# Kernel optimization log

Measured on AMD Instinct MI355X. Metric: run time of the kernel, lower is better.

## Reference

```python
import jax, jax.numpy as jnp
import numpy as np

N, B, E, H, D, L, NT = 30000, 16, 60000, 128, 64, 2, 5


def _build_graph():
    rng = np.random.default_rng(0)
    ng = N // B
    row = rng.integers(0, N, size=E)
    g = row // ng
    col = g * ng + rng.integers(0, ng, size=E)  # bonds stay within a graph
    order = np.argsort(g, kind='stable')        # sort bonds by graph id
    row, col = row[order], col[order]
    edge_index = np.stack([row, col]).astype(np.int32)
    # bond graph: bonds adjacent iff they share an atom (vectorized _build_bond_graph)
    atoms = np.concatenate([row, col])
    bonds = np.concatenate([np.arange(E), np.arange(E)])
    o2 = np.argsort(atoms, kind='stable')
    sb = bonds[o2]
    counts = np.bincount(atoms, minlength=N)
    offs = np.concatenate([[0], np.cumsum(counts)[:-1]])
    sq = counts * counts
    total = int(sq.sum())
    gid = np.repeat(np.arange(N), sq)
    poff = np.concatenate([[0], np.cumsum(sq)[:-1]])
    pos = np.arange(total) - np.repeat(poff, sq)
    c, o = counts[gid], offs[gid]
    ii, jj = pos // c, pos % c
    mask = ii != jj
    bond_edge_index = np.stack([sb[o + ii][mask], sb[o + jj][mask]]).astype(np.int32)
    batch = np.repeat(np.arange(B), ng).astype(np.int32)
    return edge_index, bond_edge_index, batch


def setup_inputs() -> dict:
    edge_index, bond_edge_index, batch = _build_graph()
    key = jax.random.key(0)
    ks = jax.random.split(key, 16)
    s = 0.05
    n = lambda k, shp: jax.random.normal(k, shp, jnp.float32) * s
    return {
        'atom_features': jax.random.normal(ks[0], (N, H), jnp.float32),
        'atom_pos': jax.random.normal(ks[1], (N, 3), jnp.float32),
        'atomic_numbers': jax.random.randint(ks[2], (N,), 1, 20, jnp.int32),
        'batch': jnp.asarray(batch),
        'edge_index': jnp.asarray(edge_index),
        'bond_edge_index': jnp.asarray(bond_edge_index),
        'iw1': n(ks[3], (2 * H, D)), 'ib1': jnp.zeros((D,), jnp.float32),
        'iw2': n(ks[4], (D, D)), 'ib2': jnp.zeros((D,), jnp.float32),
        'emb': n(ks[5], (L, NT, D)),
        'mw1': n(ks[6], (L, 3 * D, D)), 'mb1': jnp.zeros((L, D), jnp.float32),
        'mw2': n(ks[7], (L, D, D)), 'mb2': jnp.zeros((L, D), jnp.float32),
        'uw1': n(ks[8], (L, 2 * D, D)), 'ub1': jnp.zeros((L, D), jnp.float32),
        'uw2': n(ks[9], (L, D, D)), 'ub2': jnp.zeros((L, D), jnp.float32),
        'num_graphs': B,
    }


def reference(atom_features, atom_pos, iw1, ib1, iw2, ib2, emb, mw1, mb1, mw2, mb2,
              uw1, ub1, uw2, ub2, atomic_numbers, batch, edge_index, bond_edge_index,
              num_graphs):
    row, col = edge_index
    hi, hj = atom_features[row], atom_features[col]  # [E, H] gathers
    # bond_init MLP
    x = jax.nn.silu(jnp.concatenate([hi, hj], -1) @ iw1 + ib1) @ iw2 + ib2  # [E, D]
    # _classify_bonds: cosine-similarity thresholds (order matters, matches torch)
    ni = jnp.maximum(jnp.linalg.norm(hi, axis=-1), 1e-8)
    nj = jnp.maximum(jnp.linalg.norm(hj, axis=-1), 1e-8)
    sim = jnp.sum(hi * hj, -1) / (ni * nj)
    bt = jnp.where(sim > 0.8, 1, 0)
    bt = jnp.where(sim > 0.9, 2, bt)
    bt = jnp.where(sim < 0.3, 3, bt)
    src, dst = bond_edge_index  # x_j = x[src], x_i = x[dst]; aggregate at dst
    nb = x.shape[0]
    deg = jax.ops.segment_sum(jnp.ones(src.shape, jnp.float32), dst, num_segments=nb)
    denom = jnp.maximum(deg, 1.0)[:, None]  # PyG mean aggr: 0 for isolated nodes
    for l in range(mw1.shape[0]):
        te = emb[l][bt]  # [E, D] bond-type embedding
        msg_in = jnp.concatenate([x[dst], x[src], te[dst]], -1)  # [BE, 3D]
        msg = jax.nn.silu(msg_in @ mw1[l] + mb1[l]) @ mw2[l] + mb2[l]
        aggr = jax.ops.segment_sum(msg, dst, num_segments=nb) / denom
        upd_in = jnp.concatenate([aggr, x], -1)
        x = x + jax.nn.silu(upd_in @ uw1[l] + ub1[l]) @ uw2[l] + ub2[l]
    # pooling: edges are sorted by graph, so repeat_interleave == batch[row]
    bond_batch = batch[row]
    cnt = jax.ops.segment_sum(jnp.ones((nb,), jnp.float32), bond_batch, num_segments=num_graphs)
    gfeat = jax.ops.segment_sum(x, bond_batch, num_segments=num_graphs) / jnp.maximum(cnt, 1.0)[:, None]
    return x, gfeat
```

## Files before the change

### kernel.cpp

```cpp
#include <hip/hip_runtime.h>
#include <cstdint>
#include <cstddef>

#define HDIM 128
#define DDIM 64
#define NTYPES 5
#define NGRAPHS 16
#define PCHUNK 128
#define EPB 64
#define APW 8

typedef __attribute__((ext_vector_type(8))) short short8;
typedef __attribute__((ext_vector_type(4))) float f32x4;

static __device__ __forceinline__ short8 as_s8(uint4 u) {
    return __builtin_bit_cast(short8, u);
}

static __device__ __forceinline__ float silu_f(float v) {
    return v * __builtin_amdgcn_rcpf(1.0f + __expf(-v));
}

static __device__ __forceinline__ float4 ld4(const float* p) {
    return *reinterpret_cast<const float4*>(p);
}

static __device__ __forceinline__ void st4(float* p, float4 v) {
    *reinterpret_cast<float4*>(p) = v;
}

static __device__ __forceinline__ float4 add4(float4 a, float4 b) {
    return make_float4(a.x + b.x, a.y + b.y, a.z + b.z, a.w + b.w);
}

static __device__ __forceinline__ void silu_acc4(float4& s, float4 v) {
    s.x += silu_f(v.x);
    s.y += silu_f(v.y);
    s.z += silu_f(v.z);
    s.w += silu_f(v.w);
}

static __device__ __forceinline__ unsigned int bf16r(float f) {
    unsigned int u = __float_as_uint(f);
    return (u + 0x7FFFu + ((u >> 16) & 1u)) >> 16;
}
static __device__ __forceinline__ uint4 pack8(const float* f) {
    uint4 r;
    r.x = bf16r(f[0]) | (bf16r(f[1]) << 16);
    r.y = bf16r(f[2]) | (bf16r(f[3]) << 16);
    r.z = bf16r(f[4]) | (bf16r(f[5]) << 16);
    r.w = bf16r(f[6]) | (bf16r(f[7]) << 16);
    return r;
}
static __device__ __forceinline__ void unpack8(uint4 u, float4& a, float4& b) {
    a.x = __uint_as_float(u.x << 16);
    a.y = __uint_as_float(u.x & 0xFFFF0000u);
    a.z = __uint_as_float(u.y << 16);
    a.w = __uint_as_float(u.y & 0xFFFF0000u);
    b.x = __uint_as_float(u.z << 16);
    b.y = __uint_as_float(u.z & 0xFFFF0000u);
    b.z = __uint_as_float(u.w << 16);
    b.w = __uint_as_float(u.w & 0xFFFF0000u);
}

static __device__ __forceinline__ void hilo8(const float* f, uint4& h, uint4& lo) {
    h = pack8(f);
    float4 a, b;
    unpack8(h, a, b);
    float g[8] = {f[0] - a.x, f[1] - a.y, f[2] - a.z, f[3] - a.w,
                  f[4] - b.x, f[5] - b.y, f[6] - b.z, f[7] - b.w};
    lo = pack8(g);
}

static __device__ __forceinline__ int xcd_logical_block() {
    int chunk = (int)(gridDim.x >> 3);
    return (int)(blockIdx.x & 7) * chunk + (int)(blockIdx.x >> 3);
}

__global__ void __launch_bounds__(256) count_k(const int* __restrict__ bdst,
                                               int* __restrict__ cnt, int BE) {
    int i = blockIdx.x * 256 + threadIdx.x;
    if (i < BE)
        __hip_atomic_fetch_add(&cnt[bdst[i]], 1, __ATOMIC_RELAXED, __HIP_MEMORY_SCOPE_AGENT);
}

__global__ void __launch_bounds__(256) bsum_k(const int* __restrict__ cnt,
                                              int* __restrict__ bsum, int E) {
    __shared__ int red[256];
    int t = threadIdx.x;
    int i = blockIdx.x * 256 + t;
    red[t] = (i < E) ? cnt[i] : 0;
    __syncthreads();
    #pragma unroll
    for (int off = 128; off > 0; off >>= 1) {
        if (t < off) red[t] += red[t + off];
        __syncthreads();
    }
    if (t == 0) bsum[blockIdx.x] = red[0];
}

__global__ void __launch_bounds__(1024) bscan_k(const int* __restrict__ bsum,
                                                int* __restrict__ bpre, int NB) {
    __shared__ int sh[1024];
    int t = threadIdx.x;
    int v0 = (t < NB) ? bsum[t] : 0;
    sh[t] = v0;
    __syncthreads();
    for (int off = 1; off < 1024; off <<= 1) {
        int v = (t >= off) ? sh[t - off] : 0;
        __syncthreads();
        sh[t] += v;
        __syncthreads();
    }
    if (t < NB) bpre[t] = sh[t] - v0;
}

__global__ void __launch_bounds__(256) offs_k(const int* __restrict__ cnt,
                                              const int* __restrict__ bpre,
                                              int* __restrict__ offs,
                                              int* __restrict__ cursor, int E) {
    __shared__ int sh[256];
    int t = threadIdx.x;
    int i = blockIdx.x * 256 + t;
    int v0 = (i < E) ? cnt[i] : 0;
    sh[t] = v0;
    __syncthreads();
    for (int off = 1; off < 256; off <<= 1) {
        int v = (t >= off) ? sh[t - off] : 0;
        __syncthreads();
        sh[t] += v;
        __syncthreads();
    }
    int ex = sh[t] - v0 + bpre[blockIdx.x];
    if (i < E) { offs[i] = ex; cursor[i] = ex; }
    if (i == E - 1) offs[E] = ex + v0;
}

__global__ void __launch_bounds__(256) scatter_k(const int* __restrict__ bsrc,
                                                 const int* __restrict__ bdst,
                                                 int* __restrict__ cursor,
                                                 int* __restrict__ srclist, int BE) {
    int i = blockIdx.x * 256 + threadIdx.x;
    if (i < BE) {
        int d = bdst[i];
        int p = __hip_atomic_fetch_add(&cursor[d], 1, __ATOMIC_RELAXED,
                                       __HIP_MEMORY_SCOPE_AGENT);
        srclist[p] = bsrc[i];
    }
}

__global__ void __launch_bounds__(64) tt2_k(const float* __restrict__ emb,
                                            const float* __restrict__ mw1,
                                            const float* __restrict__ mb1,
                                            float* __restrict__ tt) {
    int b = blockIdx.x;
    int l = b / NTYPES, t = b % NTYPES, j = threadIdx.x;
    const float* embl = emb + (size_t)l * NTYPES * DDIM + (size_t)t * DDIM;
    const float* w1 = mw1 + (size_t)l * 192 * DDIM;
    float s = mb1[l * DDIM + j];
    #pragma unroll 8
    for (int k = 0; k < DDIM; ++k)
        s = fmaf(embl[k], w1[(HDIM + k) * DDIM + j], s);
    tt[(size_t)b * DDIM + j] = s;
}

__global__ void __launch_bounds__(64) fuse_k(const float* __restrict__ mw2,
                                             const float* __restrict__ mb2,
                                             const float* __restrict__ uw1,
                                             float* __restrict__ w2u,
                                             float* __restrict__ b2u) {
    int l = blockIdx.x >> 6, k = blockIdx.x & 63, j = threadIdx.x;
    const float* w2 = mw2 + (size_t)l * DDIM * DDIM;
    const float* u1 = uw1 + (size_t)l * 128 * DDIM;
    float s = 0.f;
    #pragma unroll 8
    for (int t = 0; t < DDIM; ++t)
        s = fmaf(w2[k * DDIM + t], u1[(size_t)t * DDIM + j], s);
    w2u[(size_t)l * DDIM * DDIM + (size_t)k * DDIM + j] = s;
    if (k == 0) {
        float b = 0.f;
        #pragma unroll 8
        for (int t = 0; t < DDIM; ++t)
            b = fmaf(mb2[l * DDIM + t], u1[(size_t)t * DDIM + j], b);
        b2u[l * DDIM + j] = b;
    }
}

__global__ void __launch_bounds__(64) packall_k(const float* __restrict__ w2u,
                                                const float* __restrict__ uw1,
                                                const float* __restrict__ uw2,
                                                const float* __restrict__ mw1,
                                                const float* __restrict__ iw2,
                                                uint4* __restrict__ fw2u,
                                                uint4* __restrict__ fu1b,
                                                uint4* __restrict__ fu2,
                                                uint4* __restrict__ fp,
                                                uint4* __restrict__ fiw2,
                                                uint4* __restrict__ fp0) {
    int b = blockIdx.x;
    int mat = b >> 3, jt = (b >> 1) & 3, ks = b & 1, l = threadIdx.x;
    const float* src;
    uint4* dst;
    switch (mat) {
        case 0: src = w2u;                         dst = fw2u;        break;
        case 1: src = w2u + 4096;                  dst = fw2u + 1024; break;
        case 2: src = uw1 + 64 * 64;               dst = fu1b;        break;
        case 3: src = uw1 + 128 * 64 + 64 * 64;    dst = fu1b + 1024; break;
        case 4: src = uw2;                         dst = fu2;         break;
        case 5: src = uw2 + 4096;                  dst = fu2 + 1024;  break;
        case 6: src = mw1 + (size_t)192 * 64;      dst = fp;          break;
        case 7: src = mw1 + (size_t)192 * 64 + 64 * 64; dst = fp + 1024; break;
        case 8: src = iw2;                         dst = fiw2;        break;
        case 9: src = mw1;                         dst = fp0;         break;
        default: src = mw1 + (size_t)64 * 64;      dst = fp0 + 1024;  break;
    }
    int k0 = ks * 32 + (l >> 4) * 8;
    int j = jt * 16 + (l & 15);
    float f[8];
    #pragma unroll
    for (int i = 0; i < 8; ++i) f[i] = src[(size_t)(k0 + i) * 64 + j];
    uint4 h, lo;
    hilo8(f, h, lo);
    size_t di = ((size_t)(jt * 2 + ks) * 64 + l) * 2;
    dst[di] = h;
    dst[di + 1] = lo;
}

static __device__ __forceinline__ int slotIdx(int row, int slot) {
    return row * 8 + (slot ^ (row & 7));
}

static __device__ __forceinline__ short8 ldFragA(const uint4* buf, int rowBase, int lane, int ks) {
    int row = rowBase + (lane & 15);
    int slot = ks * 4 + (lane >> 4);
    return as_s8(buf[slotIdx(row, slot)]);
}

static __device__ __forceinline__ void loadB(const uint4* __restrict__ frag, int jt, int lane,
                                             short8& h0, short8& h1, short8& l0, short8& l1) {
    const uint4* p0 = frag + ((size_t)(jt * 2 + 0) * 64 + lane) * 2;
    const uint4* p1 = frag + ((size_t)(jt * 2 + 1) * 64 + lane) * 2;
    h0 = as_s8(p0[0]); l0 = as_s8(p0[1]);
    h1 = as_s8(p1[0]); l1 = as_s8(p1[1]);
}

static __device__ __forceinline__ f32x4 gemm_tile(const uint4* Ahi, const uint4* Alo,
        int rowBase, int lane,
        short8 bh0, short8 bh1, short8 bl0, short8 bl1, f32x4 acc) {
    short8 ah0 = ldFragA(Ahi, rowBase, lane, 0);
    short8 ah1 = ldFragA(Ahi, rowBase, lane, 1);
    short8 al0 = ldFragA(Alo, rowBase, lane, 0);
    short8 al1 = ldFragA(Alo, rowBase, lane, 1);
    acc = __builtin_amdgcn_mfma_f32_16x16x32_bf16(ah0, bh0, acc, 0, 0, 0);
    acc = __builtin_amdgcn_mfma_f32_16x16x32_bf16(ah1, bh1, acc, 0, 0, 0);
    acc = __builtin_amdgcn_mfma_f32_16x16x32_bf16(al0, bh0, acc, 0, 0, 0);
    acc = __builtin_amdgcn_mfma_f32_16x16x32_bf16(al1, bh1, acc, 0, 0, 0);
    acc = __builtin_amdgcn_mfma_f32_16x16x32_bf16(ah0, bl0, acc, 0, 0, 0);
    acc = __builtin_amdgcn_mfma_f32_16x16x32_bf16(ah1, bl1, acc, 0, 0, 0);
    return acc;
}

__global__ void __launch_bounds__(256) atom_proj_k(
    const float* __restrict__ AF, const float* __restrict__ iw1,
    float* __restrict__ pa, float* __restrict__ qa, float* __restrict__ na, int N) {
    int lane = threadIdx.x & 63;
    int w = __builtin_amdgcn_readfirstlane((int)(threadIdx.x >> 6));
    int abase = blockIdx.x * (4 * APW) + w * APW;
    if (abase >= N) return;

    float accp[APW], accq[APW], nrm[APW];
    #pragma unroll
    for (int a = 0; a < APW; ++a) { accp[a] = 0.f; accq[a] = 0.f; nrm[a] = 0.f; }

    #pragma unroll 4
    for (int k = 0; k < HDIM; k += 4) {
        float wt[4], wb[4];
        #pragma unroll
        for (int kk = 0; kk < 4; ++kk) {
            wt[kk] = iw1[(size_t)(k + kk) * DDIM + lane];
            wb[kk] = iw1[(size_t)(HDIM + k + kk) * DDIM + lane];
        }
        #pragma unroll
        for (int a = 0; a < APW; ++a) {
            int aa = min(abase + a, N - 1);
            float4 hv = ld4(AF + (size_t)aa * HDIM + k);
            accp[a] = fmaf(hv.x, wt[0], accp[a]);
            accp[a] = fmaf(hv.y, wt[1], accp[a]);
            accp[a] = fmaf(hv.z, wt[2], accp[a]);
            accp[a] = fmaf(hv.w, wt[3], accp[a]);
            accq[a] = fmaf(hv.x, wb[0], accq[a]);
            accq[a] = fmaf(hv.y, wb[1], accq[a]);
            accq[a] = fmaf(hv.z, wb[2], accq[a]);
            accq[a] = fmaf(hv.w, wb[3], accq[a]);
            nrm[a] = fmaf(hv.x, hv.x, nrm[a]);
            nrm[a] = fmaf(hv.y, hv.y, nrm[a]);
            nrm[a] = fmaf(hv.z, hv.z, nrm[a]);
            nrm[a] = fmaf(hv.w, hv.w, nrm[a]);
        }
    }
    #pragma unroll
    for (int a = 0; a < APW; ++a) {
        int atom = abase + a;
        if (atom < N) {
            pa[(size_t)atom * DDIM + lane] = accp[a];
            qa[(size_t)atom * DDIM + lane] = accq[a];
            if (lane == 0) na[atom] = sqrtf(nrm[a]);
        }
    }
}

__global__ void __launch_bounds__(512, 4) bond_init2_k(
    const float* __restrict__ AF, const int* __restrict__ row, const int* __restrict__ col,
    const float* __restrict__ pa, const float* __restrict__ qa, const float* __restrict__ na,
    const float* __restrict__ b1, const uint4* __restrict__ fW2, const float* __restrict__ b2,
    const uint4* __restrict__ fP0,
    float* __restrict__ x, int* __restrict__ bt,
    float* __restrict__ pd, uint4* __restrict__ ps, int E) {
    __shared__ uint4 sAhi[512];
    __shared__ uint4 sAlo[512];
    __shared__ uint4 sXhi[512];
    __shared__ uint4 sXlo[512];
    int nEB = (E + EPB - 1) / EPB;
    int lb = xcd_logical_block();
    if (lb >= nEB) return;
    int tid = threadIdx.x;
    int lane = tid & 63;
    int w = __builtin_amdgcn_readfirstlane((int)(tid >> 6));
    int e0 = lb * EPB;

    {
        int dl = tid >> 3, q = tid & 7;
        int d = e0 + dl;
        bool ok = d < E;
        int dd = ok ? d : 0;
        int r = row[dd], c = col[dd];
        int jq = q * 8;

        const float* hi = AF + (size_t)r * HDIM + q * 16;
        const float* hj = AF + (size_t)c * HDIM + q * 16;
        float dt = 0.f;
        #pragma unroll
        for (int k = 0; k < 16; k += 4) {
            float4 a4 = ld4(hi + k), b4 = ld4(hj + k);
            dt += a4.x * b4.x + a4.y * b4.y + a4.z * b4.z + a4.w * b4.w;
        }
        dt += __shfl_xor(dt, 1, 64);
        dt += __shfl_xor(dt, 2, 64);
        dt += __shfl_xor(dt, 4, 64);
        if (q == 0 && ok) {
            float nr = fmaxf(na[r], 1e-8f), nc = fmaxf(na[c], 1e-8f);
            float sim = dt / (nr * nc);
            int t = 0;
            if (sim > 0.8f) t = 1;
            if (sim > 0.9f) t = 2;
            if (sim < 0.3f) t = 3;
            bt[d] = t;
        }

        const float* pr = pa + (size_t)r * DDIM + jq;
        const float* qc = qa + (size_t)c * DDIM + jq;
        float4 p0 = ld4(pr + 0), p1 = ld4(pr + 4);
        float4 q0 = ld4(qc + 0), q1 = ld4(qc + 4);
        float hv[8];
        hv[0] = silu_f(p0.x + q0.x + b1[jq + 0]);
        hv[1] = silu_f(p0.y + q0.y + b1[jq + 1]);
        hv[2] = silu_f(p0.z + q0.z + b1[jq + 2]);
        hv[3] = silu_f(p0.w + q0.w + b1[jq + 3]);
        hv[4] = silu_f(p1.x + q1.x + b1[jq + 4]);
        hv[5] = silu_f(p1.y + q1.y + b1[jq + 5]);
        hv[6] = silu_f(p1.z + q1.z + b1[jq + 6]);
        hv[7] = silu_f(p1.w + q1.w + b1[jq + 7]);
        if (!ok) {
            #pragma unroll
            for (int i = 0; i < 8; ++i) hv[i] = 0.f;
        }
        uint4 h4, l4;
        hilo8(hv, h4, l4);
        int si = slotIdx(dl, q);
        sAhi[si] = h4; sAlo[si] = l4;
    }
    int jt = w & 3, mh = w >> 2;
    short8 W2h0, W2h1, W2l0, W2l1;
    loadB(fW2, jt, lane, W2h0, W2h1, W2l0, W2l1);
    __syncthreads();

    int rb0 = mh * 32, rb1 = mh * 32 + 16;
    f32x4 z4 = {0.f, 0.f, 0.f, 0.f};
    f32x4 acc0 = z4, acc1 = z4;
    acc0 = gemm_tile(sAhi, sAlo, rb0, lane, W2h0, W2h1, W2l0, W2l1, acc0);
    acc1 = gemm_tile(sAhi, sAlo, rb1, lane, W2h0, W2h1, W2l0, W2l1, acc1);
    int j = jt * 16 + (lane & 15);
    float b2j = b2[j];
    unsigned short* hX = (unsigned short*)sXhi;
    unsigned short* lX = (unsigned short*)sXlo;
    #pragma unroll
    for (int r = 0; r < 4; ++r) {
        int rowi = rb0 + (lane >> 4) * 4 + r;
        int e = e0 + rowi;
        float xn = acc0[r] + b2j;
        if (e < E) x[(size_t)e * DDIM + j] = xn;
        unsigned int hb = bf16r(xn);
        float lov = xn - __uint_as_float(hb << 16);
        int ui = (rowi * 8 + ((j >> 3) ^ (rowi & 7))) * 8 + (j & 7);
        hX[ui] = (unsigned short)hb;
        lX[ui] = (unsigned short)bf16r(lov);
    }
    #pragma unroll
    for (int r = 0; r < 4; ++r) {
        int rowi = rb1 + (lane >> 4) * 4 + r;
        int e = e0 + rowi;
        float xn = acc1[r] + b2j;
        if (e < E) x[(size_t)e * DDIM + j] = xn;
        unsigned int hb = bf16r(xn);
        float lov = xn - __uint_as_float(hb << 16);
        int ui = (rowi * 8 + ((j >> 3) ^ (rowi & 7))) * 8 + (j & 7);
        hX[ui] = (unsigned short)hb;
        lX[ui] = (unsigned short)bf16r(lov);
    }
    __syncthreads();

    const uint4* fPw = (w < 4) ? fP0 : (fP0 + 1024);
    int jp = w & 3;
    short8 Ph0, Ph1, Pl0, Pl1;
    loadB(fPw, jp, lane, Ph0, Ph1, Pl0, Pl1);
    f32x4 q0 = z4, q1 = z4, q2 = z4, q3 = z4;
    q0 = gemm_tile(sXhi, sXlo, 0,  lane, Ph0, Ph1, Pl0, Pl1, q0);
    q1 = gemm_tile(sXhi, sXlo, 16, lane, Ph0, Ph1, Pl0, Pl1, q1);
    q2 = gemm_tile(sXhi, sXlo, 32, lane, Ph0, Ph1, Pl0, Pl1, q2);
    q3 = gemm_tile(sXhi, sXlo, 48, lane, Ph0, Ph1, Pl0, Pl1, q3);
    unsigned short* hA = (unsigned short*)sAhi;
    if (w < 4) {
        int jd = jp * 16 + (lane & 15);
        #pragma unroll
        for (int mt = 0; mt < 4; ++mt) {
            f32x4 qq = (mt == 0) ? q0 : (mt == 1) ? q1 : (mt == 2) ? q2 : q3;
            #pragma unroll
            for (int r = 0; r < 4; ++r) {
                int rowi = mt * 16 + (lane >> 4) * 4 + r;
                int e = e0 + rowi;
                if (e < E) pd[(size_t)e * DDIM + jd] = qq[r];
            }
        }
    } else {
        int js = jp * 16 + (lane & 15);
        #pragma unroll
        for (int mt = 0; mt < 4; ++mt) {
            f32x4 qq = (mt == 0) ? q0 : (mt == 1) ? q1 : (mt == 2) ? q2 : q3;
            #pragma unroll
            for (int r = 0; r < 4; ++r) {
                int rowi = mt * 16 + (lane >> 4) * 4 + r;
                int ui = (rowi * 8 + ((js >> 3) ^ (rowi & 7))) * 8 + (js & 7);
                hA[ui] = (unsigned short)bf16r(qq[r]);
            }
        }
    }
    __syncthreads();
    {
        int dl = tid >> 3, q = tid & 7;
        int d = e0 + dl;
        if (d < E) ps[(size_t)d * 8 + q] = sAhi[slotIdx(dl, q)];
    }
}

__global__ void __launch_bounds__(256) proj_k(const float* __restrict__ x,
                                              const float* __restrict__ w1 ,
                                              float* __restrict__ pd, uint4* __restrict__ ps,
                                              int E) {
    int lane = threadIdx.x & 63;
    int w = __builtin_amdgcn_readfirstlane((int)(threadIdx.x >> 6));
    int e = blockIdx.x * EPB + lane;
    bool ok = e < E;
    int eidx = ok ? e : 0;
    int j0 = w * 16;
    const float* xr = x + (size_t)eidx * DDIM;

    float apd[16], aps[16];
    #pragma unroll
    for (int jj = 0; jj < 16; ++jj) { apd[jj] = 0.f; aps[jj] = 0.f; }
    #pragma unroll 2
    for (int c = 0; c < 16; ++c) {
        float4 v = ld4(xr + c * 4);
        float xv[4] = {v.x, v.y, v.z, v.w};
        #pragma unroll
        for (int kk = 0; kk < 4; ++kk) {
            int k = c * 4 + kk;
            const float* wd = w1 + (size_t)k * DDIM + j0;
            const float* wsv = w1 + (size_t)(DDIM + k) * DDIM + j0;
            #pragma unroll
            for (int jj = 0; jj < 16; ++jj) {
                apd[jj] = fmaf(xv[kk], wd[jj], apd[jj]);
                aps[jj] = fmaf(xv[kk], wsv[jj], aps[jj]);
            }
        }
    }
    if (ok) {
        float* pr = pd + (size_t)e * DDIM + j0;
        st4(pr + 0,  make_float4(apd[0],  apd[1],  apd[2],  apd[3]));
        st4(pr + 4,  make_float4(apd[4],  apd[5],  apd[6],  apd[7]));
        st4(pr + 8,  make_float4(apd[8],  apd[9],  apd[10], apd[11]));
        st4(pr + 12, make_float4(apd[12], apd[13], apd[14], apd[15]));
        ps[(size_t)e * 8 + 2 * w + 0] = pack8(aps + 0);
        ps[(size_t)e * 8 + 2 * w + 1] = pack8(aps + 8);
    }
}

__global__ void __launch_bounds__(512, 4) layer_k(
    float* __restrict__ x, const float* __restrict__ pd, const uint4* __restrict__ ps,
    const float* __restrict__ tt_l, const int* __restrict__ bt,
    const int* __restrict__ offs, const int* __restrict__ srclist,
    const int* __restrict__ cnt,
    const uint4* __restrict__ fW2u, const float* __restrict__ b2u,
    const uint4* __restrict__ fU1b, const float* __restrict__ ub1,
    const uint4* __restrict__ fU2, const float* __restrict__ ub2,
    const uint4* __restrict__ fP ,
    float* __restrict__ pdn, uint4* __restrict__ psn, int E) {
    __shared__ uint4 sAhi[512];
    __shared__ uint4 sAlo[512];
    __shared__ uint4 sXhi[512];
    __shared__ uint4 sXlo[512];
    __shared__ float degLDS[64];
    int nEB = (E + EPB - 1) / EPB;
    int lb = xcd_logical_block();
    if (lb >= nEB) return;
    int tid = threadIdx.x;
    int lane = tid & 63;
    int w = __builtin_amdgcn_readfirstlane((int)(tid >> 6));
    int e0 = lb * EPB;

    {
        int dl = tid >> 3, q = tid & 7;
        int d = e0 + dl;
        bool ok = d < E;
        int dd = ok ? d : 0;
        int jq = q * 8;
        const float* xr = x + (size_t)dd * DDIM + jq;
        float4 xv0 = ld4(xr + 0), xv1 = ld4(xr + 4);
        int dc = cnt[dd];
        const float* pr = pd + (size_t)dd * DDIM + jq;
        const float* tp = tt_l + (size_t)bt[dd] * DDIM + jq;
        float4 b0 = add4(ld4(pr + 0), ld4(tp + 0));
        float4 b1 = add4(ld4(pr + 4), ld4(tp + 4));
        float4 s0 = make_float4(0, 0, 0, 0), s1 = s0;
        int p0 = ok ? offs[d] : 0, p1 = ok ? offs[d + 1] : 0;
        int p = p0;
        for (; p + 4 <= p1; p += 4) {
            uint4 u0 = ps[(size_t)srclist[p + 0] * 8 + q];
            uint4 u1 = ps[(size_t)srclist[p + 1] * 8 + q];
            uint4 u2 = ps[(size_t)srclist[p + 2] * 8 + q];
            uint4 u3 = ps[(size_t)srclist[p + 3] * 8 + q];
            float4 a, b;
            unpack8(u0, a, b);
            silu_acc4(s0, add4(b0, a));
            silu_acc4(s1, add4(b1, b));
            unpack8(u1, a, b);
            silu_acc4(s0, add4(b0, a));
            silu_acc4(s1, add4(b1, b));
            unpack8(u2, a, b);
            silu_acc4(s0, add4(b0, a));
            silu_acc4(s1, add4(b1, b));
            unpack8(u3, a, b);
            silu_acc4(s0, add4(b0, a));
            silu_acc4(s1, add4(b1, b));
        }
        for (; p < p1; ++p) {
            uint4 u0 = ps[(size_t)srclist[p] * 8 + q];
            float4 a, b;
            unpack8(u0, a, b);
            silu_acc4(s0, add4(b0, a));
            silu_acc4(s1, add4(b1, b));
        }
        float inv = 1.0f / fmaxf((float)dc, 1.0f);
        float sv[8] = {s0.x * inv, s0.y * inv, s0.z * inv, s0.w * inv,
                       s1.x * inv, s1.y * inv, s1.z * inv, s1.w * inv};
        float xf[8] = {xv0.x, xv0.y, xv0.z, xv0.w, xv1.x, xv1.y, xv1.z, xv1.w};
        if (!ok) {
            #pragma unroll
            for (int i = 0; i < 8; ++i) { sv[i] = 0.f; xf[i] = 0.f; }
        }
        uint4 h4, l4;
        int si = slotIdx(dl, q);
        hilo8(sv, h4, l4);
        sAhi[si] = h4; sAlo[si] = l4;
        hilo8(xf, h4, l4);
        sXhi[si] = h4; sXlo[si] = l4;
        if (q == 0) degLDS[dl] = (ok && dc > 0) ? 1.0f : 0.0f;
    }
    int jt = w & 3, mh = w >> 2;
    short8 A2h0, A2h1, A2l0, A2l1;
    short8 U1h0, U1h1, U1l0, U1l1;
    loadB(fW2u, jt, lane, A2h0, A2h1, A2l0, A2l1);
    loadB(fU1b, jt, lane, U1h0, U1h1, U1l0, U1l1);
    __syncthreads();

    int rb0 = mh * 32, rb1 = mh * 32 + 16;
    f32x4 z4 = {0.f, 0.f, 0.f, 0.f};
    f32x4 acc0 = z4, acc1 = z4;
    acc0 = gemm_tile(sAhi, sAlo, rb0, lane, A2h0, A2h1, A2l0, A2l1, acc0);
    acc0 = gemm_tile(sXhi, sXlo, rb0, lane, U1h0, U1h1, U1l0, U1l1, acc0);
    acc1 = gemm_tile(sAhi, sAlo, rb1, lane, A2h0, A2h1, A2l0, A2l1, acc1);
    acc1 = gemm_tile(sXhi, sXlo, rb1, lane, U1h0, U1h1, U1l0, U1l1, acc1);
    __syncthreads();
    int j = jt * 16 + (lane & 15);
    float ub1j = ub1[j], b2uj = b2u[j];
    unsigned short* hA = (unsigned short*)sAhi;
    unsigned short* lA = (unsigned short*)sAlo;
    #pragma unroll
    for (int r = 0; r < 4; ++r) {
        int row = rb0 + (lane >> 4) * 4 + r;
        float hv = silu_f(acc0[r] + ub1j + degLDS[row] * b2uj);
        unsigned int hb = bf16r(hv);
        float lov = hv - __uint_as_float(hb << 16);
        int ui = (row * 8 + ((j >> 3) ^ (row & 7))) * 8 + (j & 7);
        hA[ui] = (unsigned short)hb;
        lA[ui] = (unsigned short)bf16r(lov);
    }
    #pragma unroll
    for (int r = 0; r < 4; ++r) {
        int row = rb1 + (lane >> 4) * 4 + r;
        float hv = silu_f(acc1[r] + ub1j + degLDS[row] * b2uj);
        unsigned int hb = bf16r(hv);
        float lov = hv - __uint_as_float(hb << 16);
        int ui = (row * 8 + ((j >> 3) ^ (row & 7))) * 8 + (j & 7);
        hA[ui] = (unsigned short)hb;
        lA[ui] = (unsigned short)bf16r(lov);
    }
    __syncthreads();

    short8 U2h0, U2h1, U2l0, U2l1;
    loadB(fU2, jt, lane, U2h0, U2h1, U2l0, U2l1);
    f32x4 o0 = z4, o1 = z4;
    o0 = gemm_tile(sAhi, sAlo, rb0, lane, U2h0, U2h1, U2l0, U2l1, o0);
    o1 = gemm_tile(sAhi, sAlo, rb1, lane, U2h0, U2h1, U2l0, U2l1, o1);
    float ub2j = ub2[j];
    bool haveP = (fP != nullptr);
    unsigned short* hX = (unsigned short*)sXhi;
    unsigned short* lX = (unsigned short*)sXlo;
    #pragma unroll
    for (int r = 0; r < 4; ++r) {
        int row = rb0 + (lane >> 4) * 4 + r;
        int e = e0 + row;
        float xvv = (e < E) ? x[(size_t)e * DDIM + j] : 0.f;
        float xn = xvv + o0[r] + ub2j;
        if (e < E) x[(size_t)e * DDIM + j] = xn;
        if (haveP) {
            unsigned int hb = bf16r(xn);
            float lov = xn - __uint_as_float(hb << 16);
            int ui = (row * 8 + ((j >> 3) ^ (row & 7))) * 8 + (j & 7);
            hX[ui] = (unsigned short)hb;
            lX[ui] = (unsigned short)bf16r(lov);
        }
    }
    #pragma unroll
    for (int r = 0; r < 4; ++r) {
        int row = rb1 + (lane >> 4) * 4 + r;
        int e = e0 + row;
        float xvv = (e < E) ? x[(size_t)e * DDIM + j] : 0.f;
        float xn = xvv + o1[r] + ub2j;
        if (e < E) x[(size_t)e * DDIM + j] = xn;
        if (haveP) {
            unsigned int hb = bf16r(xn);
            float lov = xn - __uint_as_float(hb << 16);
            int ui = (row * 8 + ((j >> 3) ^ (row & 7))) * 8 + (j & 7);
            hX[ui] = (unsigned short)hb;
            lX[ui] = (unsigned short)bf16r(lov);
        }
    }
    if (!haveP) return;
    __syncthreads();

    const uint4* fPw = (w < 4) ? fP : (fP + 1024);
    int jp = w & 3;
    short8 Ph0, Ph1, Pl0, Pl1;
    loadB(fPw, jp, lane, Ph0, Ph1, Pl0, Pl1);
    f32x4 q0 = z4, q1 = z4, q2 = z4, q3 = z4;
    q0 = gemm_tile(sXhi, sXlo, 0,  lane, Ph0, Ph1, Pl0, Pl1, q0);
    q1 = gemm_tile(sXhi, sXlo, 16, lane, Ph0, Ph1, Pl0, Pl1, q1);
    q2 = gemm_tile(sXhi, sXlo, 32, lane, Ph0, Ph1, Pl0, Pl1, q2);
    q3 = gemm_tile(sXhi, sXlo, 48, lane, Ph0, Ph1, Pl0, Pl1, q3);
    if (w < 4) {
        int jd = jp * 16 + (lane & 15);
        #pragma unroll
        for (int mt = 0; mt < 4; ++mt) {
            f32x4 qq = (mt == 0) ? q0 : (mt == 1) ? q1 : (mt == 2) ? q2 : q3;
            #pragma unroll
            for (int r = 0; r < 4; ++r) {
                int row = mt * 16 + (lane >> 4) * 4 + r;
                int e = e0 + row;
                if (e < E) pdn[(size_t)e * DDIM + jd] = qq[r];
            }
        }
    } else {
        int js = jp * 16 + (lane & 15);
        #pragma unroll
        for (int mt = 0; mt < 4; ++mt) {
            f32x4 qq = (mt == 0) ? q0 : (mt == 1) ? q1 : (mt == 2) ? q2 : q3;
            #pragma unroll
            for (int r = 0; r < 4; ++r) {
                int row = mt * 16 + (lane >> 4) * 4 + r;
                int ui = (row * 8 + ((js >> 3) ^ (row & 7))) * 8 + (js & 7);
                hA[ui] = (unsigned short)bf16r(qq[r]);
            }
        }
    }
    __syncthreads();
    {
        int dl = tid >> 3, q = tid & 7;
        int d = e0 + dl;
        if (d < E) psn[(size_t)d * 8 + q] = sAhi[slotIdx(dl, q)];
    }
}

__global__ void __launch_bounds__(256) pool_k(
    const float* __restrict__ x, const int* __restrict__ row,
    const int* __restrict__ batch, float* __restrict__ gfeat, int E) {
    int lane = threadIdx.x & 63;
    int esub = threadIdx.x >> 6;
    int e0 = blockIdx.x * PCHUNK;
    int e1 = min(e0 + PCHUNK, E);
    float sum = 0.f;
    int cur = -1;
    for (int e = e0 + esub; e < e1; e += 4) {
        int g = batch[row[e]];
        if (g != cur) {
            if (cur >= 0)
                __hip_atomic_fetch_add(&gfeat[cur * DDIM + lane], sum,
                                       __ATOMIC_RELAXED, __HIP_MEMORY_SCOPE_AGENT);
            cur = g;
            sum = 0.f;
        }
        sum += x[(size_t)e * DDIM + lane];
    }
    if (cur >= 0)
        __hip_atomic_fetch_add(&gfeat[cur * DDIM + lane], sum,
                               __ATOMIC_RELAXED, __HIP_MEMORY_SCOPE_AGENT);
}

static __device__ __forceinline__ int lower_bound_bb(const int* __restrict__ row,
                                                     const int* __restrict__ batch,
                                                     int E, int g) {
    int lo = 0, hi = E;
    while (lo < hi) {
        int m = (lo + hi) >> 1;
        if (batch[row[m]] < g) lo = m + 1; else hi = m;
    }
    return lo;
}

__global__ void __launch_bounds__(64) pool_final_k(
    const int* __restrict__ row, const int* __restrict__ batch,
    float* __restrict__ gfeat, int E) {
    int g = blockIdx.x, j = threadIdx.x;
    int s = lower_bound_bb(row, batch, E, g);
    int t = lower_bound_bb(row, batch, E, g + 1);
    float cnt = fmaxf((float)(t - s), 1.0f);
    gfeat[g * DDIM + j] /= cnt;
}

extern "C" void kernel_launch(void* const* d_in, const int* in_sizes, int n_in,
                              void* d_out, int out_size, void* d_ws, size_t ws_size,
                              hipStream_t stream) {
    (void)n_in; (void)out_size;
    const float* AF    = (const float*)d_in[0];
    const int*   batch = (const int*)d_in[3];
    const int*   edge_index      = (const int*)d_in[4];
    const int*   bond_edge_index = (const int*)d_in[5];
    const float* iw1 = (const float*)d_in[6];
    const float* ib1 = (const float*)d_in[7];
    const float* iw2 = (const float*)d_in[8];
    const float* ib2 = (const float*)d_in[9];
    const float* emb = (const float*)d_in[10];
    const float* mw1 = (const float*)d_in[11];
    const float* mb1 = (const float*)d_in[12];
    const float* mw2 = (const float*)d_in[13];
    const float* mb2 = (const float*)d_in[14];
    const float* uw1 = (const float*)d_in[15];
    const float* ub1 = (const float*)d_in[16];
    const float* uw2 = (const float*)d_in[17];
    const float* ub2 = (const float*)d_in[18];

    const int N  = in_sizes[0] / HDIM;
    const int E  = in_sizes[4] / 2;
    const int BE = in_sizes[5] / 2;
    const int NB = (E + 255) / 256;
    const int EB = (E + EPB - 1) / EPB;
    const int AB = (N + 4 * APW - 1) / (4 * APW);
    const int EBS = ((EB + 7) / 8) * 8;
    const int PB = (E + PCHUNK - 1) / PCHUNK;

    float* xout  = (float*)d_out;
    float* gfeat = xout + (size_t)E * DDIM;

    char* w = (char*)d_ws;
    float* tt       = (float*)w;  w += sizeof(float) * 2 * NTYPES * DDIM;
    float* w2u      = (float*)w;  w += sizeof(float) * 2 * DDIM * DDIM;
    float* b2u      = (float*)w;  w += sizeof(float) * 2 * DDIM;
    w = (char*)(((uintptr_t)w + 15) & ~(uintptr_t)15);
    uint4* fW2u     = (uint4*)w;  w += 2048 * sizeof(uint4);
    uint4* fU1b     = (uint4*)w;  w += 2048 * sizeof(uint4);
    uint4* fU2      = (uint4*)w;  w += 2048 * sizeof(uint4);
    uint4* fP       = (uint4*)w;  w += 2048 * sizeof(uint4);
    uint4* fIw2     = (uint4*)w;  w += 1024 * sizeof(uint4);
    uint4* fP0      = (uint4*)w;  w += 2048 * sizeof(uint4);
    int*   cnt      = (int*)w;    w += sizeof(int) * E;
    int*   offs     = (int*)w;    w += sizeof(int) * (E + 1);
    int*   cursor   = (int*)w;    w += sizeof(int) * E;
    int*   bt       = (int*)w;    w += sizeof(int) * E;
    int*   bsum     = (int*)w;    w += sizeof(int) * 1024;
    int*   bpre     = (int*)w;    w += sizeof(int) * 1024;
    int*   srclist  = (int*)w;    w += sizeof(int) * BE;
    w = (char*)(((uintptr_t)w + 15) & ~(uintptr_t)15);
    float* pd       = (float*)w;  w += sizeof(float) * (size_t)E * DDIM;
    uint4* ps       = (uint4*)w;  w += sizeof(unsigned short) * (size_t)E * DDIM;
    float* pa       = (float*)w;  w += sizeof(float) * (size_t)N * DDIM;
    float* qa       = (float*)w;  w += sizeof(float) * (size_t)N * DDIM;
    float* na       = (float*)w;  w += sizeof(float) * (size_t)N;
    w = (char*)(((uintptr_t)w + 15) & ~(uintptr_t)15);
    float* pd2      = (float*)w;  w += sizeof(float) * (size_t)E * DDIM;
    uint4* ps2      = (uint4*)w;  w += sizeof(unsigned short) * (size_t)E * DDIM;
    bool fuse_proj = ((size_t)(w - (char*)d_ws) <= ws_size);

    const int* row  = edge_index;
    const int* col  = edge_index + E;
    const int* bsrc = bond_edge_index;
    const int* bdst = bond_edge_index + BE;

    hipMemsetAsync(cnt, 0, (size_t)E * sizeof(int), stream);
    count_k<<<(BE + 255) / 256, 256, 0, stream>>>(bdst, cnt, BE);
    bsum_k<<<NB, 256, 0, stream>>>(cnt, bsum, E);
    bscan_k<<<1, 1024, 0, stream>>>(bsum, bpre, NB);
    offs_k<<<NB, 256, 0, stream>>>(cnt, bpre, offs, cursor, E);
    scatter_k<<<(BE + 255) / 256, 256, 0, stream>>>(bsrc, bdst, cursor, srclist, BE);

    tt2_k<<<2 * NTYPES, 64, 0, stream>>>(emb, mw1, mb1, tt);
    fuse_k<<<2 * 64, 64, 0, stream>>>(mw2, mb2, uw1, w2u, b2u);
    packall_k<<<88, 64, 0, stream>>>(w2u, uw1, uw2, mw1, iw2,
                                     fW2u, fU1b, fU2, fP, fIw2, fP0);

    atom_proj_k<<<AB, 256, 0, stream>>>(AF, iw1, pa, qa, na, N);
    bond_init2_k<<<EBS, 512, 0, stream>>>(AF, row, col, pa, qa, na, ib1, fIw2, ib2,
                                          fP0, xout, bt, pd, ps, E);

    if (fuse_proj) {
        layer_k<<<EBS, 512, 0, stream>>>(
            xout, pd, ps, tt, bt, offs, srclist, cnt,
            fW2u, b2u, fU1b, ub1, fU2, ub2,
            fP, pd2, ps2, E);
        layer_k<<<EBS, 512, 0, stream>>>(
            xout, pd2, ps2, tt + NTYPES * DDIM, bt, offs, srclist, cnt,
            fW2u + 1024, b2u + DDIM, fU1b + 1024, ub1 + DDIM,
            fU2 + 1024, ub2 + DDIM,
            nullptr, nullptr, nullptr, E);
    } else {
        for (int l = 0; l < 2; ++l) {
            if (l > 0)
                proj_k<<<EB, 256, 0, stream>>>(xout, mw1 + (size_t)l * 192 * 64, pd, ps, E);
            layer_k<<<EBS, 512, 0, stream>>>(
                xout, pd, ps, tt + (size_t)l * NTYPES * DDIM, bt, offs, srclist, cnt,
                fW2u + (size_t)l * 1024, b2u + (size_t)l * DDIM,
                fU1b + (size_t)l * 1024, ub1 + (size_t)l * DDIM,
                fU2 + (size_t)l * 1024, ub2 + (size_t)l * DDIM,
                nullptr, nullptr, nullptr, E);
        }
    }

    hipMemsetAsync(gfeat, 0, NGRAPHS * DDIM * sizeof(float), stream);
    pool_k<<<PB, 256, 0, stream>>>(xout, row, batch, gfeat, E);
    pool_final_k<<<NGRAPHS, 64, 0, stream>>>(row, batch, gfeat, E);
}
```

Baseline: 319.6 us.

## Merge weight-prep kernels, use hardware bf16 pack, reuse LDS copy of x

Merges the three small weight-preparation kernels (tt2, fuse, packall) into one prep kernel that computes the W2·U1 product inline while packing, which removes two launches and the w2u scratch buffer. Replaces the software bf16 rounding in pack8 and hilo8 with the v_cvt_pk_bf16_f32 instruction. In the layer update, the residual x is rebuilt from the hi/lo bf16 copies already held in shared memory instead of being reloaded from global memory. Accumulator initialisation is also simplified. The inline W2·U1 recomputation adds redundant FMAs per block, and the hi+lo reconstruction of x may differ slightly from the fp32 value.

After: 315.2 us. About the same (-1.4%).

```diff
diff --git a/kernel.cpp b/kernel.cpp
--- a/kernel.cpp
+++ b/kernel.cpp
@@ -44,12 +44,17 @@
     unsigned int u = __float_as_uint(f);
     return (u + 0x7FFFu + ((u >> 16) & 1u)) >> 16;
 }
+static __device__ __forceinline__ unsigned int cvtpk(float a, float b) {
+    unsigned int r;
+    asm("v_cvt_pk_bf16_f32 %0, %1, %2" : "=v"(r) : "v"(a), "v"(b));
+    return r;
+}
 static __device__ __forceinline__ uint4 pack8(const float* f) {
     uint4 r;
-    r.x = bf16r(f[0]) | (bf16r(f[1]) << 16);
-    r.y = bf16r(f[2]) | (bf16r(f[3]) << 16);
-    r.z = bf16r(f[4]) | (bf16r(f[5]) << 16);
-    r.w = bf16r(f[6]) | (bf16r(f[7]) << 16);
+    r.x = cvtpk(f[0], f[1]);
+    r.y = cvtpk(f[2], f[3]);
+    r.z = cvtpk(f[4], f[5]);
+    r.w = cvtpk(f[6], f[7]);
     return r;
 }
 static __device__ __forceinline__ void unpack8(uint4 u, float4& a, float4& b) {
@@ -67,9 +72,10 @@
     h = pack8(f);
     float4 a, b;
     unpack8(h, a, b);
-    float g[8] = {f[0] - a.x, f[1] - a.y, f[2] - a.z, f[3] - a.w,
-                  f[4] - b.x, f[5] - b.y, f[6] - b.z, f[7] - b.w};
-    lo = pack8(g);
+    lo.x = cvtpk(f[0] - a.x, f[1] - a.y);
+    lo.y = cvtpk(f[2] - a.z, f[3] - a.w);
+    lo.z = cvtpk(f[4] - b.x, f[5] - b.y);
+    lo.w = cvtpk(f[6] - b.z, f[7] - b.w);
 }
 
 static __device__ __forceinline__ int xcd_logical_block() {
@@ -149,76 +155,79 @@
     }
 }
 
-__global__ void __launch_bounds__(64) tt2_k(const float* __restrict__ emb,
-                                            const float* __restrict__ mw1,
-                                            const float* __restrict__ mb1,
-                                            float* __restrict__ tt) {
-    int b = blockIdx.x;
-    int l = b / NTYPES, t = b % NTYPES, j = threadIdx.x;
-    const float* embl = emb + (size_t)l * NTYPES * DDIM + (size_t)t * DDIM;
-    const float* w1 = mw1 + (size_t)l * 192 * DDIM;
-    float s = mb1[l * DDIM + j];
-    #pragma unroll 8
-    for (int k = 0; k < DDIM; ++k)
-        s = fmaf(embl[k], w1[(HDIM + k) * DDIM + j], s);
-    tt[(size_t)b * DDIM + j] = s;
-}
-
-__global__ void __launch_bounds__(64) fuse_k(const float* __restrict__ mw2,
+__global__ void __launch_bounds__(64) prep_k(const float* __restrict__ emb,
+                                             const float* __restrict__ mw1,
+                                             const float* __restrict__ mb1,
+                                             const float* __restrict__ mw2,
                                              const float* __restrict__ mb2,
                                              const float* __restrict__ uw1,
-                                             float* __restrict__ w2u,
-                                             float* __restrict__ b2u) {
-    int l = blockIdx.x >> 6, k = blockIdx.x & 63, j = threadIdx.x;
-    const float* w2 = mw2 + (size_t)l * DDIM * DDIM;
-    const float* u1 = uw1 + (size_t)l * 128 * DDIM;
-    float s = 0.f;
-    #pragma unroll 8
-    for (int t = 0; t < DDIM; ++t)
-        s = fmaf(w2[k * DDIM + t], u1[(size_t)t * DDIM + j], s);
-    w2u[(size_t)l * DDIM * DDIM + (size_t)k * DDIM + j] = s;
-    if (k == 0) {
-        float b = 0.f;
+                                             const float* __restrict__ uw2,
+                                             const float* __restrict__ iw2,
+                                             float* __restrict__ tt,
+                                             float* __restrict__ b2u,
+                                             uint4* __restrict__ fw2u,
+                                             uint4* __restrict__ fu1b,
+                                             uint4* __restrict__ fu2,
+                                             uint4* __restrict__ fp,
+                                             uint4* __restrict__ fiw2,
+                                             uint4* __restrict__ fp0) {
+    int b = blockIdx.x;
+    int l = threadIdx.x;
+    if (b < 10) {
+        int ll = b / NTYPES, t = b % NTYPES;
+        const float* embl = emb + (size_t)ll * NTYPES * DDIM + (size_t)t * DDIM;
+        const float* w1 = mw1 + (size_t)ll * 192 * DDIM;
+        float s = mb1[ll * DDIM + l];
+        #pragma unroll 8
+        for (int k = 0; k < DDIM; ++k)
+            s = fmaf(embl[k], w1[(HDIM + k) * DDIM + l], s);
+        tt[(size_t)b * DDIM + l] = s;
+        return;
+    }
+    if (b < 12) {
+        int ll = b - 10;
+        const float* u1 = uw1 + (size_t)ll * 128 * DDIM;
+        float s = 0.f;
         #pragma unroll 8
         for (int t = 0; t < DDIM; ++t)
-            b = fmaf(mb2[l * DDIM + t], u1[(size_t)t * DDIM + j], b);
-        b2u[l * DDIM + j] = b;
-    }
-}
-
-__global__ void __launch_bounds__(64) packall_k(const float* __restrict__ w2u,
-                                                const float* __restrict__ uw1,
-                                                const float* __restrict__ uw2,
-                                                const float* __restrict__ mw1,
-                                                const float* __restrict__ iw2,
-                                                uint4* __restrict__ fw2u,
-                                                uint4* __restrict__ fu1b,
-                                                uint4* __restrict__ fu2,
-                                                uint4* __restrict__ fp,
-                                                uint4* __restrict__ fiw2,
-                                                uint4* __restrict__ fp0) {
-    int b = blockIdx.x;
-    int mat = b >> 3, jt = (b >> 1) & 3, ks = b & 1, l = threadIdx.x;
-    const float* src;
-    uint4* dst;
-    switch (mat) {
-        case 0: src = w2u;                         dst = fw2u;        break;
-        case 1: src = w2u + 4096;                  dst = fw2u + 1024; break;
-        case 2: src = uw1 + 64 * 64;               dst = fu1b;        break;
-        case 3: src = uw1 + 128 * 64 + 64 * 64;    dst = fu1b + 1024; break;
-        case 4: src = uw2;                         dst = fu2;         break;
-        case 5: src = uw2 + 4096;                  dst = fu2 + 1024;  break;
-        case 6: src = mw1 + (size_t)192 * 64;      dst = fp;          break;
-        case 7: src = mw1 + (size_t)192 * 64 + 64 * 64; dst = fp + 1024; break;
-        case 8: src = iw2;                         dst = fiw2;        break;
-        case 9: src = mw1;                         dst = fp0;         break;
-        default: src = mw1 + (size_t)64 * 64;      dst = fp0 + 1024;  break;
-    }
+            s = fmaf(mb2[ll * DDIM + t], u1[(size_t)t * DDIM + l], s);
+        b2u[ll * DDIM + l] = s;
+        return;
+    }
+    int pb = b - 12;
+    int mat = pb >> 3, jt = (pb >> 1) & 3, ks = pb & 1;
     int k0 = ks * 32 + (l >> 4) * 8;
     int j = jt * 16 + (l & 15);
     float f[8];
-    #pragma unroll
-    for (int i = 0; i < 8; ++i) f[i] = src[(size_t)(k0 + i) * 64 + j];
+    uint4* dst;
+    if (mat <= 1) {
+        const float* w2 = mw2 + (size_t)mat * DDIM * DDIM;
+        const float* u1 = uw1 + (size_t)mat * 128 * DDIM;
+        #pragma unroll
+        for (int i = 0; i < 8; ++i) {
+            float s = 0.f;
+            #pragma unroll 8
+            for (int t = 0; t < DDIM; ++t)
+                s = fmaf(w2[(size_t)(k0 + i) * DDIM + t], u1[(size_t)t * DDIM + j], s);
+            f[i] = s;
+        }
+        dst = fw2u + (size_t)mat * 1024;
+    } else {
+        const float* src;
+        switch (mat) {
+            case 2:  src = uw1 + 64 * 64;                   dst = fu1b;        break;
+            case 3:  src = uw1 + 128 * 64 + 64 * 64;        dst = fu1b + 1024; break;
+            case 4:  src = uw2;                             dst = fu2;         break;
+            case 5:  src = uw2 + 4096;                      dst = fu2 + 1024;  break;
+            case 6:  src = mw1 + (size_t)192 * 64;          dst = fp;          break;
+            case 7:  src = mw1 + (size_t)192 * 64 + 64 * 64; dst = fp + 1024;  break;
+            case 8:  src = iw2;                             dst = fiw2;        break;
+            case 9:  src = mw1;                             dst = fp0;         break;
+            default: src = mw1 + (size_t)64 * 64;           dst = fp0 + 1024;  break;
+        }
+        #pragma unroll
+        for (int i = 0; i < 8; ++i) f[i] = src[(size_t)(k0 + i) * DDIM + j];
+    }
     uint4 h, lo;
     hilo8(f, h, lo);
     size_t di = ((size_t)(jt * 2 + ks) * 64 + l) * 2;
@@ -386,9 +395,8 @@
 
     int rb0 = mh * 32, rb1 = mh * 32 + 16;
     f32x4 z4 = {0.f, 0.f, 0.f, 0.f};
-    f32x4 acc0 = z4, acc1 = z4;
-    acc0 = gemm_tile(sAhi, sAlo, rb0, lane, W2h0, W2h1, W2l0, W2l1, acc0);
-    acc1 = gemm_tile(sAhi, sAlo, rb1, lane, W2h0, W2h1, W2l0, W2l1, acc1);
+    f32x4 acc0 = gemm_tile(sAhi, sAlo, rb0, lane, W2h0, W2h1, W2l0, W2l1, z4);
+    f32x4 acc1 = gemm_tile(sAhi, sAlo, rb1, lane, W2h0, W2h1, W2l0, W2l1, z4);
     int j = jt * 16 + (lane & 15);
     float b2j = b2[j];
     unsigned short* hX = (unsigned short*)sXhi;
@@ -423,11 +431,10 @@
     int jp = w & 3;
     short8 Ph0, Ph1, Pl0, Pl1;
     loadB(fPw, jp, lane, Ph0, Ph1, Pl0, Pl1);
-    f32x4 q0 = z4, q1 = z4, q2 = z4, q3 = z4;
-    q0 = gemm_tile(sXhi, sXlo, 0,  lane, Ph0, Ph1, Pl0, Pl1, q0);
-    q1 = gemm_tile(sXhi, sXlo, 16, lane, Ph0, Ph1, Pl0, Pl1, q1);
-    q2 = gemm_tile(sXhi, sXlo, 32, lane, Ph0, Ph1, Pl0, Pl1, q2);
-    q3 = gemm_tile(sXhi, sXlo, 48, lane, Ph0, Ph1, Pl0, Pl1, q3);
+    f32x4 q0 = gemm_tile(sXhi, sXlo, 0,  lane, Ph0, Ph1, Pl0, Pl1, z4);
+    f32x4 q1 = gemm_tile(sXhi, sXlo, 16, lane, Ph0, Ph1, Pl0, Pl1, z4);
+    f32x4 q2 = gemm_tile(sXhi, sXlo, 32, lane, Ph0, Ph1, Pl0, Pl1, z4);
+    f32x4 q3 = gemm_tile(sXhi, sXlo, 48, lane, Ph0, Ph1, Pl0, Pl1, z4);
     unsigned short* hA = (unsigned short*)sAhi;
     if (w < 4) {
         int jd = jp * 16 + (lane & 15);
@@ -628,9 +635,8 @@
 
     short8 U2h0, U2h1, U2l0, U2l1;
     loadB(fU2, jt, lane, U2h0, U2h1, U2l0, U2l1);
-    f32x4 o0 = z4, o1 = z4;
-    o0 = gemm_tile(sAhi, sAlo, rb0, lane, U2h0, U2h1, U2l0, U2l1, o0);
-    o1 = gemm_tile(sAhi, sAlo, rb1, lane, U2h0, U2h1, U2l0, U2l1, o1);
+    f32x4 o0 = gemm_tile(sAhi, sAlo, rb0, lane, U2h0, U2h1, U2l0, U2l1, z4);
+    f32x4 o1 = gemm_tile(sAhi, sAlo, rb1, lane, U2h0, U2h1, U2l0, U2l1, z4);
     float ub2j = ub2[j];
     bool haveP = (fP != nullptr);
     unsigned short* hX = (unsigned short*)sXhi;
@@ -639,13 +645,14 @@
     for (int r = 0; r < 4; ++r) {
         int row = rb0 + (lane >> 4) * 4 + r;
         int e = e0 + row;
-        float xvv = (e < E) ? x[(size_t)e * DDIM + j] : 0.f;
+        int ui = (row * 8 + ((j >> 3) ^ (row & 7))) * 8 + (j & 7);
+        float xvv = __uint_as_float((unsigned int)hX[ui] << 16)
+                  + __uint_as_float((unsigned int)lX[ui] << 16);
         float xn = xvv + o0[r] + ub2j;
         if (e < E) x[(size_t)e * DDIM + j] = xn;
         if (haveP) {
             unsigned int hb = bf16r(xn);
             float lov = xn - __uint_as_float(hb << 16);
-            int ui = (row * 8 + ((j >> 3) ^ (row & 7))) * 8 + (j & 7);
             hX[ui] = (unsigned short)hb;
             lX[ui] = (unsigned short)bf16r(lov);
         }
@@ -654,13 +661,14 @@
     for (int r = 0; r < 4; ++r) {
         int row = rb1 + (lane >> 4) * 4 + r;
         int e = e0 + row;
-        float xvv = (e < E) ? x[(size_t)e * DDIM + j] : 0.f;
+        int ui = (row * 8 + ((j >> 3) ^ (row & 7))) * 8 + (j & 7);
+        float xvv = __uint_as_float((unsigned int)hX[ui] << 16)
+                  + __uint_as_float((unsigned int)lX[ui] << 16);
         float xn = xvv + o1[r] + ub2j;
         if (e < E) x[(size_t)e * DDIM + j] = xn;
         if (haveP) {
             unsigned int hb = bf16r(xn);
             float lov = xn - __uint_as_float(hb << 16);
-            int ui = (row * 8 + ((j >> 3) ^ (row & 7))) * 8 + (j & 7);
             hX[ui] = (unsigned short)hb;
             lX[ui] = (unsigned short)bf16r(lov);
         }
@@ -672,11 +680,10 @@
     int jp = w & 3;
     short8 Ph0, Ph1, Pl0, Pl1;
     loadB(fPw, jp, lane, Ph0, Ph1, Pl0, Pl1);
-    f32x4 q0 = z4, q1 = z4, q2 = z4, q3 = z4;
-    q0 = gemm_tile(sXhi, sXlo, 0,  lane, Ph0, Ph1, Pl0, Pl1, q0);
-    q1 = gemm_tile(sXhi, sXlo, 16, lane, Ph0, Ph1, Pl0, Pl1, q1);
-    q2 = gemm_tile(sXhi, sXlo, 32, lane, Ph0, Ph1, Pl0, Pl1, q2);
-    q3 = gemm_tile(sXhi, sXlo, 48, lane, Ph0, Ph1, Pl0, Pl1, q3);
+    f32x4 q0 = gemm_tile(sXhi, sXlo, 0,  lane, Ph0, Ph1, Pl0, Pl1, z4);
+    f32x4 q1 = gemm_tile(sXhi, sXlo, 16, lane, Ph0, Ph1, Pl0, Pl1, z4);
+    f32x4 q2 = gemm_tile(sXhi, sXlo, 32, lane, Ph0, Ph1, Pl0, Pl1, z4);
+    f32x4 q3 = gemm_tile(sXhi, sXlo, 48, lane, Ph0, Ph1, Pl0, Pl1, z4);
     if (w < 4) {
         int jd = jp * 16 + (lane & 15);
         #pragma unroll
@@ -792,7 +799,6 @@
 
     char* w = (char*)d_ws;
     float* tt       = (float*)w;  w += sizeof(float) * 2 * NTYPES * DDIM;
-    float* w2u      = (float*)w;  w += sizeof(float) * 2 * DDIM * DDIM;
     float* b2u      = (float*)w;  w += sizeof(float) * 2 * DDIM;
     w = (char*)(((uintptr_t)w + 15) & ~(uintptr_t)15);
     uint4* fW2u     = (uint4*)w;  w += 2048 * sizeof(uint4);
@@ -831,10 +837,8 @@
     offs_k<<<NB, 256, 0, stream>>>(cnt, bpre, offs, cursor, E);
     scatter_k<<<(BE + 255) / 256, 256, 0, stream>>>(bsrc, bdst, cursor, srclist, BE);
 
-    tt2_k<<<2 * NTYPES, 64, 0, stream>>>(emb, mw1, mb1, tt);
-    fuse_k<<<2 * 64, 64, 0, stream>>>(mw2, mb2, uw1, w2u, b2u);
-    packall_k<<<88, 64, 0, stream>>>(w2u, uw1, uw2, mw1, iw2,
-                                     fW2u, fU1b, fU2, fP, fIw2, fP0);
+    prep_k<<<100, 64, 0, stream>>>(emb, mw1, mb1, mw2, mb2, uw1, uw2, iw2,
+                                   tt, b2u, fW2u, fU1b, fU2, fP, fIw2, fP0);
 
     atom_proj_k<<<AB, 256, 0, stream>>>(AF, iw1, pa, qa, na, N);
     bond_init2_k<<<EBS, 512, 0, stream>>>(AF, row, col, pa, qa, na, ib1, fIw2, ib2,
```
